# Optimization experiments

Measured on AMD Instinct MI355X. Metric: run time of the kernel, lower is better.

Reference implementation:

```python
import jax, jax.numpy as jnp
import numpy as np
import math

HIDDEN = 1024
HEADS = 16
HEAD_DIM = HIDDEN // HEADS
B, S = 2, 2048


def _xavier(key, shape):
    fan_in, fan_out = shape[1], shape[0]
    limit = math.sqrt(6.0 / (fan_in + fan_out))
    return jax.random.uniform(key, shape, jnp.float32, -limit, limit)


def setup_inputs() -> dict:
    key = jax.random.key(0)
    ks = jax.random.split(key, 5)
    x = jax.random.normal(ks[0], (B, S, HIDDEN), jnp.float32)
    # torch Linear stores weight as [out, in]; y = x @ W.T + b
    Wq = _xavier(ks[1], (HIDDEN, HIDDEN))
    Wk = _xavier(ks[2], (HIDDEN, HIDDEN))
    Wv = _xavier(ks[3], (HIDDEN, HIDDEN))
    Wo = _xavier(ks[4], (HIDDEN, HIDDEN))
    bq = jnp.zeros((HIDDEN,), jnp.float32)
    bk = jnp.zeros((HIDDEN,), jnp.float32)
    bv = jnp.zeros((HIDDEN,), jnp.float32)
    bo = jnp.zeros((HIDDEN,), jnp.float32)
    return {"x": x, "Wq": Wq, "bq": bq, "Wk": Wk, "bk": bk,
            "Wv": Wv, "bv": bv, "Wo": Wo, "bo": bo}


def reference(x, Wq, bq, Wk, bk, Wv, bv, Wo, bo):
    b, s, d = x.shape
    h, hd = HEADS, HEAD_DIM
    q = (x @ Wq.T + bq).reshape(b, s, h, hd).transpose(0, 2, 1, 3)  # [b,h,s,hd]
    k = (x @ Wk.T + bk).reshape(b, s, h, hd).transpose(0, 2, 1, 3)
    v = (x @ Wv.T + bv).reshape(b, s, h, hd).transpose(0, 2, 1, 3)
    scores = jnp.einsum('bhqd,bhkd->bhqk', q, k) / math.sqrt(hd)
    causal = jnp.tril(jnp.ones((s, s), bool))
    scores = jnp.where(causal, scores, -jnp.inf)
    attn = jax.nn.softmax(scores, axis=-1)
    out = jnp.einsum('bhqk,bhkd->bhqd', attn, v)  # [b,h,s,hd]
    out = out.transpose(0, 2, 1, 3).reshape(b, s, d)
    return out @ Wo.T + bo
```

## Files before the change

kernel.cpp:

```cpp
#include <hip/hip_runtime.h>
#include <hip/hip_bf16.h>


typedef __hip_bfloat16 bf16;
typedef __attribute__((ext_vector_type(8))) short short8;
typedef __attribute__((ext_vector_type(4))) short short4v;
typedef __attribute__((ext_vector_type(4))) float f32x4;

#define MFMA16(a, b, c) __builtin_amdgcn_mfma_f32_16x16x32_bf16((a), (b), (c), 0, 0, 0)

__device__ __forceinline__ void load_lds16(const void* g, void* l) {
  __builtin_amdgcn_global_load_lds(
      (const __attribute__((address_space(1))) void*)g,
      (__attribute__((address_space(3))) void*)l, 16, 0, 0);
}

__global__ __launch_bounds__(256) void cvt_kernel(
    const float* __restrict__ x, const float* __restrict__ wq,
    const float* __restrict__ wk, const float* __restrict__ wv,
    const float* __restrict__ wo, bf16* __restrict__ xb, bf16* __restrict__ wqb,
    bf16* __restrict__ wkb, bf16* __restrict__ wvb, bf16* __restrict__ wob) {
  const int seg = blockIdx.y;
  const float* src;
  bf16* dst;
  int n;
  if (seg == 0)      { src = x;  dst = xb;  n = 4194304; }
  else if (seg == 1) { src = wq; dst = wqb; n = 1048576; }
  else if (seg == 2) { src = wk; dst = wkb; n = 1048576; }
  else if (seg == 3) { src = wv; dst = wvb; n = 1048576; }
  else               { src = wo; dst = wob; n = 1048576; }
  const int i = (blockIdx.x * 256 + threadIdx.x) * 4;
  if (i >= n) return;
  const float4 v = *(const float4*)(src + i);
  short4v p;
  ((bf16*)&p)[0] = __float2bfloat16(v.x);
  ((bf16*)&p)[1] = __float2bfloat16(v.y);
  ((bf16*)&p)[2] = __float2bfloat16(v.z);
  ((bf16*)&p)[3] = __float2bfloat16(v.w);
  *(short4v*)(dst + i) = p;
}

template <int BM, typename OutT, bool TRANS>
__device__ __forceinline__ void gemm_body(const bf16* __restrict__ X,
                                          const bf16* __restrict__ W,
                                          const float* __restrict__ bias,
                                          OutT* __restrict__ Y, float scale) {
  constexpr int K = 1024, N = 1024;
  constexpr int MI = BM / 32;
  __shared__ bf16 As[BM * 64];
  __shared__ bf16 Bs[128 * 64];
  const int t = threadIdx.x;
  const int lane = t & 63, w = t >> 6;
  const int quad = lane >> 4, r = lane & 15;
  const int m0 = blockIdx.y * BM, n0 = blockIdx.x * 128;
  const int wm = w >> 1, wn = w & 1;

  f32x4 acc[MI][4] = {};

  for (int k0 = 0; k0 < K; k0 += 64) {
    __syncthreads();
#pragma unroll
    for (int p = 0; p < BM / 32; ++p) {
      const int c = p * 256 + w * 64 + lane;
      const int row = c >> 3;
      const int scb = (c & 7) ^ (row & 7);
      load_lds16(X + (size_t)(m0 + row) * K + k0 + scb * 8, As + c * 8);
    }
#pragma unroll
    for (int p = 0; p < 4; ++p) {
      const int c = p * 256 + w * 64 + lane;
      const int row = c >> 3;
      const int scb = (c & 7) ^ (row & 7);
      load_lds16(W + (size_t)(n0 + row) * K + k0 + scb * 8, Bs + c * 8);
    }
    __syncthreads();
    short8 af[MI][2], bfr[4][2];
#pragma unroll
    for (int ks = 0; ks < 2; ++ks) {
#pragma unroll
      for (int i = 0; i < MI; ++i) {
        const int ra = wm * (MI * 16) + i * 16 + r;
        af[i][ks] = *(const short8*)(As + ra * 64 +
                                     (((ks * 4 + quad) ^ (ra & 7)) * 8));
      }
#pragma unroll
      for (int j = 0; j < 4; ++j) {
        const int rb = wn * 64 + j * 16 + r;
        bfr[j][ks] = *(const short8*)(Bs + rb * 64 +
                                      (((ks * 4 + quad) ^ (rb & 7)) * 8));
      }
    }
#pragma unroll
    for (int ks = 0; ks < 2; ++ks)
#pragma unroll
      for (int i = 0; i < MI; ++i)
#pragma unroll
        for (int j = 0; j < 4; ++j)
          acc[i][j] = MFMA16(af[i][ks], bfr[j][ks], acc[i][j]);
  }
#pragma unroll
  for (int i = 0; i < MI; ++i) {
    const int m = m0 + wm * (MI * 16) + i * 16 + quad * 4;
#pragma unroll
    for (int j = 0; j < 4; ++j) {
      const int n = n0 + wn * 64 + j * 16 + r;
      const float bv = bias[n];
      if constexpr (TRANS) {
        short4v pk;
#pragma unroll
        for (int g = 0; g < 4; ++g)
          ((bf16*)&pk)[g] = __float2bfloat16((acc[i][j][g] + bv) * scale);
        *(short4v*)((bf16*)Y + (size_t)n * 4096 + m) = pk;
      } else {
#pragma unroll
        for (int g = 0; g < 4; ++g) {
          const float val = (acc[i][j][g] + bv) * scale;
          if constexpr (__is_same(OutT, float))
            Y[(size_t)(m + g) * N + n] = val;
          else
            Y[(size_t)(m + g) * N + n] = __float2bfloat16(val);
        }
      }
    }
  }
}

#define QSCALE 0.18033688f

__global__ __launch_bounds__(256) void qkv_kernel(
    const bf16* __restrict__ x, const bf16* __restrict__ Wq,
    const float* __restrict__ bq, const bf16* __restrict__ Wk,
    const float* __restrict__ bk, const bf16* __restrict__ Wv,
    const float* __restrict__ bv, bf16* Qb, bf16* Kb, bf16* Vtg) {
  if (blockIdx.z == 0)      gemm_body<64, bf16, false>(x, Wq, bq, Qb, QSCALE);
  else if (blockIdx.z == 1) gemm_body<64, bf16, false>(x, Wk, bk, Kb, 1.0f);
  else                      gemm_body<64, bf16, true >(x, Wv, bv, Vtg, 1.0f);
}

__global__ __launch_bounds__(256) void proj_kernel(const bf16* __restrict__ X,
                                                   const bf16* __restrict__ W,
                                                   const float* __restrict__ bias,
                                                   float* __restrict__ Y) {
  gemm_body<64, float, false>(X, W, bias, Y, 1.0f);
}

__global__ __launch_bounds__(256) void attn_kernel(const bf16* __restrict__ Qb,
                                                   const bf16* __restrict__ Kb,
                                                   const bf16* __restrict__ Vtg,
                                                   bf16* __restrict__ Ob) {
  const int pair = blockIdx.x, h = blockIdx.y, b = blockIdx.z;
  const int t = threadIdx.x;
  const int lane = t & 63, w = t >> 6;
  const int quad = lane >> 4, r = lane & 15;

  __shared__ bf16 Ks[128 * 64];
  __shared__ bf16 Vt[64 * 128];
  __shared__ bf16 Pl[4][16 * 128];

#pragma unroll 1
  for (int sel = 0; sel < 2; ++sel) {
    const int j = sel ? (31 - pair) : pair;
    const int qrow = j * 64 + w * 16 + r;

    short8 qf[2];
#pragma unroll
    for (int ks = 0; ks < 2; ++ks)
      qf[ks] = *(const short8*)(Qb + (size_t)(b * 2048 + qrow) * 1024 + h * 64 +
                                ks * 32 + quad * 8);

    f32x4 o[4] = {};
    float lsum = 0.f;

    const int nkt = j / 2 + 1;
    for (int kt = 0; kt < nkt; ++kt) {
      const int k0 = kt * 128;
      __syncthreads();
#pragma unroll
      for (int p = 0; p < 4; ++p) {
        const int c = p * 256 + w * 64 + lane;
        const int row = c >> 3;
        const int scb = (c & 7) ^ (row & 7);
        load_lds16(Kb + (size_t)(b * 2048 + k0 + row) * 1024 + h * 64 + scb * 8,
                   Ks + c * 8);
      }
#pragma unroll
      for (int p = 0; p < 4; ++p) {
        const int c = p * 256 + w * 64 + lane;
        const int row = c >> 4;
        const int scb = (c & 15) ^ (row & 15);
        load_lds16(Vtg + (size_t)(h * 64 + row) * 4096 + b * 2048 + k0 + scb * 8,
                   Vt + c * 8);
      }
      __syncthreads();

      f32x4 st[8] = {};
#pragma unroll
      for (int ks = 0; ks < 2; ++ks) {
        short8 kf[8];
#pragma unroll
        for (int mt = 0; mt < 8; ++mt) {
          const int key = mt * 16 + r;
          kf[mt] = *(const short8*)(Ks + key * 64 +
                                    (((ks * 4 + quad) ^ (key & 7)) * 8));
        }
#pragma unroll
        for (int mt = 0; mt < 8; ++mt) st[mt] = MFMA16(kf[mt], qf[ks], st[mt]);
      }

      if (kt == nkt - 1) {
#pragma unroll
        for (int mt = 0; mt < 8; ++mt)
#pragma unroll
          for (int g = 0; g < 4; ++g) {
            const int key = k0 + mt * 16 + quad * 4 + g;
            if (key > qrow) st[mt][g] = -1e30f;
          }
      }

#pragma unroll
      for (int mt = 0; mt < 8; ++mt) {
        bf16 pk[4];
#pragma unroll
        for (int g = 0; g < 4; ++g) {
          const float p = exp2f(st[mt][g]);
          pk[g] = __float2bfloat16(p);
          lsum += p;
        }
        const int key8 = mt * 2 + (quad >> 1);
        const int off = r * 128 + ((key8 ^ (r & 15)) * 8) + (quad & 1) * 4;
        *(short4v*)(&Pl[w][off]) = *(const short4v*)pk;
      }

      asm volatile("s_waitcnt lgkmcnt(0)" ::: "memory");

#pragma unroll
      for (int ks = 0; ks < 4; ++ks) {
        short8 vf[4], pf;
#pragma unroll
        for (int mt = 0; mt < 4; ++mt) {
          const int d = mt * 16 + r;
          vf[mt] = *(const short8*)(Vt + d * 128 +
                                    (((ks * 4 + quad) ^ (d & 15)) * 8));
        }
        pf = *(const short8*)(Pl[w] + r * 128 +
                              (((ks * 4 + quad) ^ (r & 15)) * 8));
#pragma unroll
        for (int mt = 0; mt < 4; ++mt) o[mt] = MFMA16(vf[mt], pf, o[mt]);
      }
    }

    lsum += __shfl_xor(lsum, 16);
    lsum += __shfl_xor(lsum, 32);
    const float inv = 1.f / lsum;

#pragma unroll
    for (int mt = 0; mt < 4; ++mt) {
      const int d0 = mt * 16 + quad * 4;
      short4v pk;
#pragma unroll
      for (int g = 0; g < 4; ++g)
        ((bf16*)&pk)[g] = __float2bfloat16(o[mt][g] * inv);
      *(short4v*)(Ob + (size_t)(b * 2048 + qrow) * 1024 + h * 64 + d0) = pk;
    }
  }
}

extern "C" void kernel_launch(void* const* d_in, const int* in_sizes, int n_in,
                              void* d_out, int out_size, void* d_ws, size_t ws_size,
                              hipStream_t stream) {
  const float* x  = (const float*)d_in[0];
  const float* Wq = (const float*)d_in[1];
  const float* bq = (const float*)d_in[2];
  const float* Wk = (const float*)d_in[3];
  const float* bk = (const float*)d_in[4];
  const float* Wv = (const float*)d_in[5];
  const float* bv = (const float*)d_in[6];
  const float* Wo = (const float*)d_in[7];
  const float* bo = (const float*)d_in[8];
  float* out = (float*)d_out;

  bf16* xb  = (bf16*)d_ws;
  bf16* wqb = xb  + (size_t)4096 * 1024;
  bf16* wkb = wqb + (size_t)1024 * 1024;
  bf16* wvb = wkb + (size_t)1024 * 1024;
  bf16* wob = wvb + (size_t)1024 * 1024;
  bf16* Qb  = wob + (size_t)1024 * 1024;
  bf16* Kb  = Qb  + (size_t)4096 * 1024;
  bf16* Vtg = Kb  + (size_t)4096 * 1024;
  bf16* Ob  = Vtg + (size_t)4096 * 1024;
  const size_t need = ((size_t)4096 * 1024 * 5 + (size_t)1024 * 1024 * 4) * 2;
  if (ws_size < need) return;

  cvt_kernel<<<dim3(4096, 5), 256, 0, stream>>>(x, Wq, Wk, Wv, Wo,
                                                xb, wqb, wkb, wvb, wob);
  qkv_kernel<<<dim3(8, 64, 3), 256, 0, stream>>>(xb, wqb, bq, wkb, bk, wvb, bv,
                                                 Qb, Kb, Vtg);
  attn_kernel<<<dim3(16, 16, 2), 256, 0, stream>>>(Qb, Kb, Vtg, Ob);
  proj_kernel<<<dim3(8, 64, 1), 256, 0, stream>>>(Ob, wob, bo, out);
}
```

Baseline: 192.7 us.

## Fuse QKV weights into one 128x128-tile GEMM and trim conversion and attention overheads

Weights are converted into one concatenated buffer, and the QKV projection becomes a single GEMM over a 3072-wide output with 128x128 tiles instead of 64x128, which doubles the reuse of each loaded X tile. The cvt kernel launches only the blocks it needs and uses paired bf16 conversions. Attention precomputes its global and LDS load addresses outside the key loop and uses packed bf16x2 conversions. Larger tiles raise register use and halve the QKV block count, which may lower occupancy.

New measurement: 189.9 us. No clear change (-1.4%).

```diff
diff --git a/kernel.cpp b/kernel.cpp
--- a/kernel.cpp
+++ b/kernel.cpp
@@ -15,52 +15,136 @@
       (__attribute__((address_space(3))) void*)l, 16, 0, 0);
 }
 
+#define QSCALE 0.18033688f
+
 __global__ __launch_bounds__(256) void cvt_kernel(
     const float* __restrict__ x, const float* __restrict__ wq,
     const float* __restrict__ wk, const float* __restrict__ wv,
-    const float* __restrict__ wo, bf16* __restrict__ xb, bf16* __restrict__ wqb,
-    bf16* __restrict__ wkb, bf16* __restrict__ wvb, bf16* __restrict__ wob) {
-  const int seg = blockIdx.y;
+    const float* __restrict__ wo, bf16* __restrict__ xb,
+    bf16* __restrict__ wcat) {
+  const int bx = blockIdx.x;
   const float* src;
   bf16* dst;
-  int n;
-  if (seg == 0)      { src = x;  dst = xb;  n = 4194304; }
-  else if (seg == 1) { src = wq; dst = wqb; n = 1048576; }
-  else if (seg == 2) { src = wk; dst = wkb; n = 1048576; }
-  else if (seg == 3) { src = wv; dst = wvb; n = 1048576; }
-  else               { src = wo; dst = wob; n = 1048576; }
-  const int i = (blockIdx.x * 256 + threadIdx.x) * 4;
-  if (i >= n) return;
+  int ib;
+  if (bx < 4096) { src = x; dst = xb; ib = bx; }
+  else {
+    const int wseg = (bx - 4096) >> 10;
+    ib = (bx - 4096) & 1023;
+    src = wseg == 0 ? wq : wseg == 1 ? wk : wseg == 2 ? wv : wo;
+    dst = wcat + (size_t)wseg * 1048576;
+  }
+  const int i = (ib * 256 + threadIdx.x) * 4;
   const float4 v = *(const float4*)(src + i);
   short4v p;
-  ((bf16*)&p)[0] = __float2bfloat16(v.x);
-  ((bf16*)&p)[1] = __float2bfloat16(v.y);
-  ((bf16*)&p)[2] = __float2bfloat16(v.z);
-  ((bf16*)&p)[3] = __float2bfloat16(v.w);
+  *(__hip_bfloat162*)&p = __float22bfloat162_rn(float2{v.x, v.y});
+  *((__hip_bfloat162*)&p + 1) = __float22bfloat162_rn(float2{v.z, v.w});
   *(short4v*)(dst + i) = p;
 }
 
-template <int BM, typename OutT, bool TRANS>
-__device__ __forceinline__ void gemm_body(const bf16* __restrict__ X,
-                                          const bf16* __restrict__ W,
-                                          const float* __restrict__ bias,
-                                          OutT* __restrict__ Y, float scale) {
-  constexpr int K = 1024, N = 1024;
-  constexpr int MI = BM / 32;
-  __shared__ bf16 As[BM * 64];
+__global__ __launch_bounds__(256) void qkv_kernel(
+    const bf16* __restrict__ x, const bf16* __restrict__ Wcat,
+    const float* __restrict__ bq, const float* __restrict__ bk,
+    const float* __restrict__ bv, bf16* __restrict__ Qb,
+    bf16* __restrict__ Kb, bf16* __restrict__ Vtg) {
+  constexpr int K = 1024;
+  __shared__ bf16 As[128 * 64];
   __shared__ bf16 Bs[128 * 64];
   const int t = threadIdx.x;
   const int lane = t & 63, w = t >> 6;
   const int quad = lane >> 4, r = lane & 15;
-  const int m0 = blockIdx.y * BM, n0 = blockIdx.x * 128;
+  const int m0 = blockIdx.y * 128;
+  const int ncol = blockIdx.x * 128;
+  const int seg = ncol >> 10;
+  const int n0 = ncol & 1023;
   const int wm = w >> 1, wn = w & 1;
 
-  f32x4 acc[MI][4] = {};
+  f32x4 acc[4][4] = {};
 
   for (int k0 = 0; k0 < K; k0 += 64) {
     __syncthreads();
 #pragma unroll
-    for (int p = 0; p < BM / 32; ++p) {
+    for (int p = 0; p < 4; ++p) {
+      const int c = p * 256 + w * 64 + lane;
+      const int row = c >> 3;
+      const int scb = (c & 7) ^ (row & 7);
+      load_lds16(x + (size_t)(m0 + row) * K + k0 + scb * 8, As + c * 8);
+    }
+#pragma unroll
+    for (int p = 0; p < 4; ++p) {
+      const int c = p * 256 + w * 64 + lane;
+      const int row = c >> 3;
+      const int scb = (c & 7) ^ (row & 7);
+      load_lds16(Wcat + (size_t)(ncol + row) * K + k0 + scb * 8, Bs + c * 8);
+    }
+    __syncthreads();
+    short8 af[4][2], bfr[4][2];
+#pragma unroll
+    for (int ks = 0; ks < 2; ++ks) {
+#pragma unroll
+      for (int i = 0; i < 4; ++i) {
+        const int ra = wm * 64 + i * 16 + r;
+        af[i][ks] = *(const short8*)(As + ra * 64 +
+                                     (((ks * 4 + quad) ^ (ra & 7)) * 8));
+        const int rb = wn * 64 + i * 16 + r;
+        bfr[i][ks] = *(const short8*)(Bs + rb * 64 +
+                                      (((ks * 4 + quad) ^ (rb & 7)) * 8));
+      }
+    }
+#pragma unroll
+    for (int ks = 0; ks < 2; ++ks)
+#pragma unroll
+      for (int i = 0; i < 4; ++i)
+#pragma unroll
+        for (int j = 0; j < 4; ++j)
+          acc[i][j] = MFMA16(af[i][ks], bfr[j][ks], acc[i][j]);
+  }
+
+  const float* bias = seg == 0 ? bq : seg == 1 ? bk : bv;
+  const float scale = seg == 0 ? QSCALE : 1.0f;
+  bf16* dst01 = seg == 0 ? Qb : Kb;
+#pragma unroll
+  for (int i = 0; i < 4; ++i) {
+    const int m = m0 + wm * 64 + i * 16 + quad * 4;
+#pragma unroll
+    for (int j = 0; j < 4; ++j) {
+      const int nn = n0 + wn * 64 + j * 16 + r;
+      const float bv_ = bias[nn];
+      if (seg == 2) {
+        short4v pk;
+        *(__hip_bfloat162*)&pk = __float22bfloat162_rn(
+            float2{acc[i][j][0] + bv_, acc[i][j][1] + bv_});
+        *((__hip_bfloat162*)&pk + 1) = __float22bfloat162_rn(
+            float2{acc[i][j][2] + bv_, acc[i][j][3] + bv_});
+        *(short4v*)(Vtg + (size_t)nn * 4096 + m) = pk;
+      } else {
+#pragma unroll
+        for (int g = 0; g < 4; ++g)
+          dst01[(size_t)(m + g) * 1024 + nn] =
+              __float2bfloat16((acc[i][j][g] + bv_) * scale);
+      }
+    }
+  }
+}
+
+__global__ __launch_bounds__(256) void proj_kernel(const bf16* __restrict__ X,
+                                                   const bf16* __restrict__ W,
+                                                   const float* __restrict__ bias,
+                                                   float* __restrict__ Y) {
+  constexpr int K = 1024, N = 1024;
+  __shared__ bf16 As[64 * 64];
+  __shared__ bf16 Bs[128 * 64];
+  const int t = threadIdx.x;
+  const int lane = t & 63, w = t >> 6;
+  const int quad = lane >> 4, r = lane & 15;
+  const int m0 = blockIdx.y * 64, n0 = blockIdx.x * 128;
+  const int wm = w >> 1, wn = w & 1;
+
+  f32x4 acc[2][4] = {};
+
+  for (int k0 = 0; k0 < K; k0 += 64) {
+    __syncthreads();
+#pragma unroll
+    for (int p = 0; p < 2; ++p) {
       const int c = p * 256 + w * 64 + lane;
       const int row = c >> 3;
       const int scb = (c & 7) ^ (row & 7);
@@ -74,12 +158,12 @@
       load_lds16(W + (size_t)(n0 + row) * K + k0 + scb * 8, Bs + c * 8);
     }
     __syncthreads();
-    short8 af[MI][2], bfr[4][2];
+    short8 af[2][2], bfr[4][2];
 #pragma unroll
     for (int ks = 0; ks < 2; ++ks) {
 #pragma unroll
-      for (int i = 0; i < MI; ++i) {
-        const int ra = wm * (MI * 16) + i * 16 + r;
+      for (int i = 0; i < 2; ++i) {
+        const int ra = wm * 32 + i * 16 + r;
         af[i][ks] = *(const short8*)(As + ra * 64 +
                                      (((ks * 4 + quad) ^ (ra & 7)) * 8));
       }
@@ -93,55 +177,23 @@
 #pragma unroll
     for (int ks = 0; ks < 2; ++ks)
 #pragma unroll
-      for (int i = 0; i < MI; ++i)
+      for (int i = 0; i < 2; ++i)
 #pragma unroll
         for (int j = 0; j < 4; ++j)
           acc[i][j] = MFMA16(af[i][ks], bfr[j][ks], acc[i][j]);
   }
 #pragma unroll
-  for (int i = 0; i < MI; ++i) {
-    const int m = m0 + wm * (MI * 16) + i * 16 + quad * 4;
+  for (int i = 0; i < 2; ++i) {
+    const int m = m0 + wm * 32 + i * 16 + quad * 4;
 #pragma unroll
     for (int j = 0; j < 4; ++j) {
       const int n = n0 + wn * 64 + j * 16 + r;
       const float bv = bias[n];
-      if constexpr (TRANS) {
-        short4v pk;
-#pragma unroll
-        for (int g = 0; g < 4; ++g)
-          ((bf16*)&pk)[g] = __float2bfloat16((acc[i][j][g] + bv) * scale);
-        *(short4v*)((bf16*)Y + (size_t)n * 4096 + m) = pk;
-      } else {
-#pragma unroll
-        for (int g = 0; g < 4; ++g) {
-          const float val = (acc[i][j][g] + bv) * scale;
-          if constexpr (__is_same(OutT, float))
-            Y[(size_t)(m + g) * N + n] = val;
-          else
-            Y[(size_t)(m + g) * N + n] = __float2bfloat16(val);
-        }
-      }
-    }
-  }
-}
-
-#define QSCALE 0.18033688f
-
-__global__ __launch_bounds__(256) void qkv_kernel(
-    const bf16* __restrict__ x, const bf16* __restrict__ Wq,
-    const float* __restrict__ bq, const bf16* __restrict__ Wk,
-    const float* __restrict__ bk, const bf16* __restrict__ Wv,
-    const float* __restrict__ bv, bf16* Qb, bf16* Kb, bf16* Vtg) {
-  if (blockIdx.z == 0)      gemm_body<64, bf16, false>(x, Wq, bq, Qb, QSCALE);
-  else if (blockIdx.z == 1) gemm_body<64, bf16, false>(x, Wk, bk, Kb, 1.0f);
-  else                      gemm_body<64, bf16, true >(x, Wv, bv, Vtg, 1.0f);
-}
-
-__global__ __launch_bounds__(256) void proj_kernel(const bf16* __restrict__ X,
-                                                   const bf16* __restrict__ W,
-                                                   const float* __restrict__ bias,
-                                                   float* __restrict__ Y) {
-  gemm_body<64, float, false>(X, W, bias, Y, 1.0f);
+#pragma unroll
+      for (int g = 0; g < 4; ++g)
+        Y[(size_t)(m + g) * N + n] = acc[i][j][g] + bv;
+    }
+  }
 }
 
 __global__ __launch_bounds__(256) void attn_kernel(const bf16* __restrict__ Qb,
@@ -157,6 +209,17 @@
   __shared__ bf16 Vt[64 * 128];
   __shared__ bf16 Pl[4][16 * 128];
 
+  int rowK[4], scbK[4], rowV[4], scbV[4];
+  bf16 *klds[4], *vlds[4];
+#pragma unroll
+  for (int p = 0; p < 4; ++p) {
+    const int c = p * 256 + w * 64 + lane;
+    rowK[p] = c >> 3;  scbK[p] = (c & 7) ^ (rowK[p] & 7);
+    rowV[p] = c >> 4;  scbV[p] = (c & 15) ^ (rowV[p] & 15);
+    klds[p] = Ks + c * 8;
+    vlds[p] = Vt + c * 8;
+  }
+
 #pragma unroll 1
   for (int sel = 0; sel < 2; ++sel) {
     const int j = sel ? (31 - pair) : pair;
@@ -168,6 +231,13 @@
       qf[ks] = *(const short8*)(Qb + (size_t)(b * 2048 + qrow) * 1024 + h * 64 +
                                 ks * 32 + quad * 8);
 
+    const bf16 *kp[4], *vp[4];
+#pragma unroll
+    for (int p = 0; p < 4; ++p) {
+      kp[p] = Kb + (size_t)(b * 2048 + rowK[p]) * 1024 + h * 64 + scbK[p] * 8;
+      vp[p] = Vtg + (size_t)(h * 64 + rowV[p]) * 4096 + b * 2048 + scbV[p] * 8;
+    }
+
     f32x4 o[4] = {};
     float lsum = 0.f;
 
@@ -176,21 +246,11 @@
       const int k0 = kt * 128;
       __syncthreads();
 #pragma unroll
-      for (int p = 0; p < 4; ++p) {
-        const int c = p * 256 + w * 64 + lane;
-        const int row = c >> 3;
-        const int scb = (c & 7) ^ (row & 7);
-        load_lds16(Kb + (size_t)(b * 2048 + k0 + row) * 1024 + h * 64 + scb * 8,
-                   Ks + c * 8);
-      }
-#pragma unroll
-      for (int p = 0; p < 4; ++p) {
-        const int c = p * 256 + w * 64 + lane;
-        const int row = c >> 4;
-        const int scb = (c & 15) ^ (row & 15);
-        load_lds16(Vtg + (size_t)(h * 64 + row) * 4096 + b * 2048 + k0 + scb * 8,
-                   Vt + c * 8);
-      }
+      for (int p = 0; p < 4; ++p) load_lds16(kp[p], klds[p]);
+#pragma unroll
+      for (int p = 0; p < 4; ++p) load_lds16(vp[p], vlds[p]);
+#pragma unroll
+      for (int p = 0; p < 4; ++p) { kp[p] += 128 * 1024; vp[p] += 128; }
       __syncthreads();
 
       f32x4 st[8] = {};
@@ -219,16 +279,15 @@
 
 #pragma unroll
       for (int mt = 0; mt < 8; ++mt) {
-        bf16 pk[4];
-#pragma unroll
-        for (int g = 0; g < 4; ++g) {
-          const float p = exp2f(st[mt][g]);
-          pk[g] = __float2bfloat16(p);
-          lsum += p;
-        }
+        const float p0 = exp2f(st[mt][0]), p1 = exp2f(st[mt][1]);
+        const float p2 = exp2f(st[mt][2]), p3 = exp2f(st[mt][3]);
+        lsum += (p0 + p1) + (p2 + p3);
+        short4v pk;
+        *(__hip_bfloat162*)&pk = __float22bfloat162_rn(float2{p0, p1});
+        *((__hip_bfloat162*)&pk + 1) = __float22bfloat162_rn(float2{p2, p3});
         const int key8 = mt * 2 + (quad >> 1);
         const int off = r * 128 + ((key8 ^ (r & 15)) * 8) + (quad & 1) * 4;
-        *(short4v*)(&Pl[w][off]) = *(const short4v*)pk;
+        *(short4v*)(&Pl[w][off]) = pk;
       }
 
       asm volatile("s_waitcnt lgkmcnt(0)" ::: "memory");
@@ -257,9 +316,10 @@
     for (int mt = 0; mt < 4; ++mt) {
       const int d0 = mt * 16 + quad * 4;
       short4v pk;
-#pragma unroll
-      for (int g = 0; g < 4; ++g)
-        ((bf16*)&pk)[g] = __float2bfloat16(o[mt][g] * inv);
+      *(__hip_bfloat162*)&pk = __float22bfloat162_rn(
+          float2{o[mt][0] * inv, o[mt][1] * inv});
+      *((__hip_bfloat162*)&pk + 1) = __float22bfloat162_rn(
+          float2{o[mt][2] * inv, o[mt][3] * inv});
       *(short4v*)(Ob + (size_t)(b * 2048 + qrow) * 1024 + h * 64 + d0) = pk;
     }
   }
@@ -279,22 +339,19 @@
   const float* bo = (const float*)d_in[8];
   float* out = (float*)d_out;
 
-  bf16* xb  = (bf16*)d_ws;
-  bf16* wqb = xb  + (size_t)4096 * 1024;
-  bf16* wkb = wqb + (size_t)1024 * 1024;
-  bf16* wvb = wkb + (size_t)1024 * 1024;
-  bf16* wob = wvb + (size_t)1024 * 1024;
-  bf16* Qb  = wob + (size_t)1024 * 1024;
-  bf16* Kb  = Qb  + (size_t)4096 * 1024;
-  bf16* Vtg = Kb  + (size_t)4096 * 1024;
-  bf16* Ob  = Vtg + (size_t)4096 * 1024;
+  bf16* xb   = (bf16*)d_ws;
+  bf16* wcat = xb + (size_t)4096 * 1024;
+  bf16* wob  = wcat + (size_t)3 * 1024 * 1024;
+  bf16* Qb   = wcat + (size_t)4 * 1024 * 1024;
+  bf16* Kb   = Qb  + (size_t)4096 * 1024;
+  bf16* Vtg  = Kb  + (size_t)4096 * 1024;
+  bf16* Ob   = Vtg + (size_t)4096 * 1024;
   const size_t need = ((size_t)4096 * 1024 * 5 + (size_t)1024 * 1024 * 4) * 2;
   if (ws_size < need) return;
 
-  cvt_kernel<<<dim3(4096, 5), 256, 0, stream>>>(x, Wq, Wk, Wv, Wo,
-                                                xb, wqb, wkb, wvb, wob);
-  qkv_kernel<<<dim3(8, 64, 3), 256, 0, stream>>>(xb, wqb, bq, wkb, bk, wvb, bv,
-                                                 Qb, Kb, Vtg);
+  cvt_kernel<<<8192, 256, 0, stream>>>(x, Wq, Wk, Wv, Wo, xb, wcat);
+  qkv_kernel<<<dim3(24, 32), 256, 0, stream>>>(xb, wcat, bq, bk, bv,
+                                               Qb, Kb, Vtg);
   attn_kernel<<<dim3(16, 16, 2), 256, 0, stream>>>(Qb, Kb, Vtg, Ob);
-  proj_kernel<<<dim3(8, 64, 1), 256, 0, stream>>>(Ob, wob, bo, out);
-}
+  proj_kernel<<<dim3(8, 64), 256, 0, stream>>>(Ob, wob, bo, out);
+}
```
